# Performance work log

Hardware: AMD Instinct MI355X
Metric: run time of the kernel (lower is better)

## Reference

```python
import jax, jax.numpy as jnp
import numpy as np

B, S, D = 16, 2048, 128

def setup_inputs() -> dict:
    key = jax.random.key(0)
    kq, kk, kv = jax.random.split(key, 3)
    queries = jax.random.normal(kq, (B, S, D), dtype=jnp.float32)
    keys = jax.random.normal(kk, (B, S, D), dtype=jnp.float32)
    values = jax.random.normal(kv, (B, S, D), dtype=jnp.float32)
    return {"queries": queries, "keys": keys, "values": values}

def reference(queries, keys, values):
    # scores: [B, S, S] = Q @ K^T / sqrt(D)
    d = queries.shape[-1]
    scores = jnp.einsum('bqd,bkd->bqk', queries, keys) / jnp.float32(np.sqrt(d))
    attn = jax.nn.softmax(scores, axis=-1)
    # dropout_rate=0.0 -> identity
    out = jnp.einsum('bqk,bkd->bqd', attn, values)
    return out
```

## Files before the change

kernel.cpp:

```cpp
#include <hip/hip_runtime.h>
#include <hip/hip_bf16.h>

#define BATCH 16
#define SEQ   2048
#define DIM   128
#define KTILE 64
#define NIT   (SEQ / KTILE)
#define QT    128
#define SCALE 0.08838834764831845f

typedef __bf16 bf16_t;
typedef __bf16 bf16x8 __attribute__((ext_vector_type(8)));
typedef __bf16 bf16x4 __attribute__((ext_vector_type(4)));
typedef float  f32x4  __attribute__((ext_vector_type(4)));

#define KSTR 136

__device__ __forceinline__ int rho(int s) {
    return (s & 32) | ((s & 4) << 2) | (((s >> 3) & 3) << 2) | (s & 3);
}
__device__ __forceinline__ int swz(int row) {
    return (row & 7) ^ ((row >> 2) & 7);
}

__global__ __launch_bounds__(512, 2)
void attn_fwd(const float* __restrict__ Qg, const float* __restrict__ Kg,
              const float* __restrict__ Vg, float* __restrict__ Og)
{
    __shared__ __align__(16) bf16_t sK [2][KTILE][KSTR];
    __shared__ __align__(16) bf16_t sVt[2][DIM][64];

    const int tid  = threadIdx.x;
    const int wave = tid >> 6;
    const int lane = tid & 63;
    const int l16  = lane & 15;
    const int g    = lane >> 4;
    const bool is_comp = (wave < 4);

    const int bid   = blockIdx.x;
    const int batch = ((bid & 7) << 1) | ((bid >> 7) & 1);
    const int qtile = (bid >> 3) & 15;
    const int q0    = qtile * QT + wave * 32;

    const float* Kb = Kg + (size_t)batch * SEQ * DIM;
    const float* Vb = Vg + (size_t)batch * SEQ * DIM;

    bf16x8 qf[2][4];
    if (is_comp) {
        #pragma unroll
        for (int h = 0; h < 2; ++h) {
            const float* qp =
                Qg + ((size_t)batch * SEQ + q0 + h * 16 + l16) * DIM + g * 8;
            #pragma unroll
            for (int c = 0; c < 4; ++c) {
                const float4 u = *reinterpret_cast<const float4*>(qp + c * 32);
                const float4 v = *reinterpret_cast<const float4*>(qp + c * 32 + 4);
                bf16x8 f;
                f[0] = (bf16_t)(u.x * SCALE); f[1] = (bf16_t)(u.y * SCALE);
                f[2] = (bf16_t)(u.z * SCALE); f[3] = (bf16_t)(u.w * SCALE);
                f[4] = (bf16_t)(v.x * SCALE); f[5] = (bf16_t)(v.y * SCALE);
                f[6] = (bf16_t)(v.z * SCALE); f[7] = (bf16_t)(v.w * SCALE);
                qf[h][c] = f;
            }
        }
    }

    const int p    = tid & 255;
    const int krow = p >> 3;
    const int kch  = p & 7;
    const int vkg  = p >> 5;
    const int vd4  = p & 31;

    float4 ka[2][2][2];
    float4 va[2][4];

    auto load_tile = [&](int k0) {
        #pragma unroll
        for (int r = 0; r < 2; ++r) {
            #pragma unroll
            for (int i = 0; i < 2; ++i) {
                const float* pp =
                    Kb + (size_t)(k0 + krow + r * 32) * DIM + kch * 8 + i * 64;
                ka[r][i][0] = *reinterpret_cast<const float4*>(pp);
                ka[r][i][1] = *reinterpret_cast<const float4*>(pp + 4);
            }
            #pragma unroll
            for (int j = 0; j < 4; ++j)
                va[r][j] = *reinterpret_cast<const float4*>(
                    Vb + (size_t)(k0 + (vkg + r * 8) * 4 + j) * DIM + vd4 * 4);
        }
    };
    auto write_tile = [&](int buf) {
        #pragma unroll
        for (int r = 0; r < 2; ++r) {
            const int row = krow + r * 32;
            #pragma unroll
            for (int i = 0; i < 2; ++i) {
                const float* a = reinterpret_cast<const float*>(&ka[r][i][0]);
                bf16x8 w;
                #pragma unroll
                for (int e = 0; e < 8; ++e) w[e] = (bf16_t)a[e];
                *reinterpret_cast<bf16x8*>(&sK[buf][rho(row)][kch * 8 + i * 64]) = w;
            }
            const int kg = vkg + r * 8;
            #pragma unroll
            for (int dd = 0; dd < 4; ++dd) {
                const int vrow = vd4 * 4 + dd;
                const int col = (((kg >> 1) ^ swz(vrow)) << 3) + ((kg & 1) << 2);
                bf16x4 w;
                w[0] = (bf16_t)va[r][0][dd]; w[1] = (bf16_t)va[r][1][dd];
                w[2] = (bf16_t)va[r][2][dd]; w[3] = (bf16_t)va[r][3][dd];
                *reinterpret_cast<bf16x4*>(&sVt[buf][vrow][col]) = w;
            }
        }
    };

    const f32x4 vzero = {0.f, 0.f, 0.f, 0.f};
    f32x4 o[2][8];
    #pragma unroll
    for (int h = 0; h < 2; ++h)
        #pragma unroll
        for (int i = 0; i < 8; ++i) o[h][i] = vzero;
    float lsum[2] = {0.f, 0.f};

    if (!is_comp) {
        load_tile(0);
        write_tile(0);
        load_tile(KTILE);
    }

    for (int it = 0; it < NIT; ++it) {
        __syncthreads();

        if (!is_comp) {
            if (it + 1 < NIT) {
                write_tile((it + 1) & 1);
                if (it + 2 < NIT) load_tile((it + 2) * KTILE);
            }
            continue;
        }

        const int cur = it & 1;

        f32x4 sc[2][4];
        #pragma unroll
        for (int ksb = 0; ksb < 4; ++ksb) { sc[0][ksb] = vzero; sc[1][ksb] = vzero; }
        #pragma unroll
        for (int c = 0; c < 4; ++c) {
            #pragma unroll
            for (int ksb = 0; ksb < 4; ++ksb) {
                bf16x8 kf = *reinterpret_cast<const bf16x8*>(
                    &sK[cur][ksb * 16 + l16][c * 32 + g * 8]);
                sc[0][ksb] = __builtin_amdgcn_mfma_f32_16x16x32_bf16(
                    kf, qf[0][c], sc[0][ksb], 0, 0, 0);
                sc[1][ksb] = __builtin_amdgcn_mfma_f32_16x16x32_bf16(
                    kf, qf[1][c], sc[1][ksb], 0, 0, 0);
            }
        }

        float pe[2][16];
        #pragma unroll
        for (int h = 0; h < 2; ++h) {
            #pragma unroll
            for (int ksb = 0; ksb < 4; ++ksb) {
                #pragma unroll
                for (int r = 0; r < 4; ++r) {
                    const float pv = __expf(sc[h][ksb][r]);
                    pe[h][ksb * 4 + r] = pv;
                    lsum[h] += pv;
                }
            }
        }
        bf16x8 pb[2][2];
        #pragma unroll
        for (int h = 0; h < 2; ++h) {
            #pragma unroll
            for (int c2 = 0; c2 < 2; ++c2) {
                bf16x8 t;
                #pragma unroll
                for (int jj = 0; jj < 8; ++jj)
                    t[jj] = (bf16_t)pe[h][(2 * c2 + (jj >> 2)) * 4 + (jj & 3)];
                pb[h][c2] = t;
            }
        }

        #pragma unroll
        for (int n0 = 0; n0 < 8; ++n0) {
            const int row = n0 * 16 + l16;
            #pragma unroll
            for (int c2 = 0; c2 < 2; ++c2) {
                bf16x8 vf = *reinterpret_cast<const bf16x8*>(
                    &sVt[cur][row][((c2 * 4 + g) ^ swz(row)) << 3]);
                o[0][n0] = __builtin_amdgcn_mfma_f32_16x16x32_bf16(
                    vf, pb[0][c2], o[0][n0], 0, 0, 0);
                o[1][n0] = __builtin_amdgcn_mfma_f32_16x16x32_bf16(
                    vf, pb[1][c2], o[1][n0], 0, 0, 0);
            }
        }
    }

    if (is_comp) {
        #pragma unroll
        for (int h = 0; h < 2; ++h) {
            float l = lsum[h];
            l += __shfl_xor(l, 16);
            l += __shfl_xor(l, 32);
            const float inv = 1.f / l;
            float* op = Og + ((size_t)batch * SEQ + q0 + h * 16 + l16) * DIM + g * 4;
            #pragma unroll
            for (int n0 = 0; n0 < 8; ++n0) {
                float4 st = { o[h][n0][0] * inv, o[h][n0][1] * inv,
                              o[h][n0][2] * inv, o[h][n0][3] * inv };
                *reinterpret_cast<float4*>(op + n0 * 16) = st;
            }
        }
    }
}

extern "C" void kernel_launch(void* const* d_in, const int* in_sizes, int n_in,
                              void* d_out, int out_size, void* d_ws, size_t ws_size,
                              hipStream_t stream) {
    const float* Q = (const float*)d_in[0];
    const float* K = (const float*)d_in[1];
    const float* V = (const float*)d_in[2];
    float* O = (float*)d_out;
    dim3 grid(BATCH * SEQ / QT);
    dim3 block(512);
    hipLaunchKernelGGL(attn_fwd, grid, block, 0, stream, Q, K, V, O);
}
```

Measured before the change: 127.8 us.

## Quad-buffer K/V tiles, process two tiles per barrier, use exp2 with folded log2e

Shared-memory K/V staging grows from double to quadruple buffering. Producer waves now load and convert two tiles per sync step, and consumer waves process two tiles between barriers, which halves the number of __syncthreads. The softmax scale now folds in log2(e) so exp2f can replace __expf, the row-sum accumulation uses a tree reduction, and s_setprio raises priority around the MFMA blocks. LDS use doubles to about 136KB per block, which may hurt occupancy against the launch_bounds(512,2) target.

```diff
diff --git a/kernel.cpp b/kernel.cpp
--- a/kernel.cpp
+++ b/kernel.cpp
@@ -6,8 +6,9 @@
 #define DIM   128
 #define KTILE 64
 #define NIT   (SEQ / KTILE)
+#define NITP  (NIT / 2)
 #define QT    128
-#define SCALE 0.08838834764831845f
+#define SCALE2 (0.08838834764831845f * 1.4426950408889634f)
 
 typedef __bf16 bf16_t;
 typedef __bf16 bf16x8 __attribute__((ext_vector_type(8)));
@@ -27,8 +28,8 @@
 void attn_fwd(const float* __restrict__ Qg, const float* __restrict__ Kg,
               const float* __restrict__ Vg, float* __restrict__ Og)
 {
-    __shared__ __align__(16) bf16_t sK [2][KTILE][KSTR];
-    __shared__ __align__(16) bf16_t sVt[2][DIM][64];
+    __shared__ __align__(16) bf16_t sK [4][KTILE][KSTR];
+    __shared__ __align__(16) bf16_t sVt[4][DIM][64];
 
     const int tid  = threadIdx.x;
     const int wave = tid >> 6;
@@ -56,10 +57,10 @@
                 const float4 u = *reinterpret_cast<const float4*>(qp + c * 32);
                 const float4 v = *reinterpret_cast<const float4*>(qp + c * 32 + 4);
                 bf16x8 f;
-                f[0] = (bf16_t)(u.x * SCALE); f[1] = (bf16_t)(u.y * SCALE);
-                f[2] = (bf16_t)(u.z * SCALE); f[3] = (bf16_t)(u.w * SCALE);
-                f[4] = (bf16_t)(v.x * SCALE); f[5] = (bf16_t)(v.y * SCALE);
-                f[6] = (bf16_t)(v.z * SCALE); f[7] = (bf16_t)(v.w * SCALE);
+                f[0] = (bf16_t)(u.x * SCALE2); f[1] = (bf16_t)(u.y * SCALE2);
+                f[2] = (bf16_t)(u.z * SCALE2); f[3] = (bf16_t)(u.w * SCALE2);
+                f[4] = (bf16_t)(v.x * SCALE2); f[5] = (bf16_t)(v.y * SCALE2);
+                f[6] = (bf16_t)(v.z * SCALE2); f[7] = (bf16_t)(v.w * SCALE2);
                 qf[h][c] = f;
             }
         }
@@ -71,12 +72,11 @@
     const int vkg  = p >> 5;
     const int vd4  = p & 31;
 
-    float4 ka[2][2][2];
-    float4 va[2][4];
-
-    auto load_tile = [&](int k0) {
-        #pragma unroll
-        for (int r = 0; r < 2; ++r) {
+    auto stage = [&](int k0, int buf) {
+        float4 ka[2][2][2];
+        float4 va[2][4];
+        #pragma unroll
+        for (int r = 0; r < 2; ++r)
             #pragma unroll
             for (int i = 0; i < 2; ++i) {
                 const float* pp =
@@ -84,13 +84,12 @@
                 ka[r][i][0] = *reinterpret_cast<const float4*>(pp);
                 ka[r][i][1] = *reinterpret_cast<const float4*>(pp + 4);
             }
+        #pragma unroll
+        for (int r = 0; r < 2; ++r)
             #pragma unroll
             for (int j = 0; j < 4; ++j)
                 va[r][j] = *reinterpret_cast<const float4*>(
                     Vb + (size_t)(k0 + (vkg + r * 8) * 4 + j) * DIM + vd4 * 4);
-        }
-    };
-    auto write_tile = [&](int buf) {
         #pragma unroll
         for (int r = 0; r < 2; ++r) {
             const int row = krow + r * 32;
@@ -117,85 +116,99 @@
 
     const f32x4 vzero = {0.f, 0.f, 0.f, 0.f};
     f32x4 o[2][8];
-    #pragma unroll
-    for (int h = 0; h < 2; ++h)
-        #pragma unroll
-        for (int i = 0; i < 8; ++i) o[h][i] = vzero;
-    float lsum[2] = {0.f, 0.f};
+    float lsum[2];
+    if (is_comp) {
+        #pragma unroll
+        for (int h = 0; h < 2; ++h) {
+            #pragma unroll
+            for (int i = 0; i < 8; ++i) o[h][i] = vzero;
+            lsum[h] = 0.f;
+        }
+    }
 
     if (!is_comp) {
-        load_tile(0);
-        write_tile(0);
-        load_tile(KTILE);
-    }
-
-    for (int it = 0; it < NIT; ++it) {
+        stage(0, 0);
+        __builtin_amdgcn_sched_barrier(0);
+        stage(KTILE, 1);
+    }
+
+    for (int t = 0; t < NITP; ++t) {
         __syncthreads();
 
         if (!is_comp) {
-            if (it + 1 < NIT) {
-                write_tile((it + 1) & 1);
-                if (it + 2 < NIT) load_tile((it + 2) * KTILE);
+            if (t + 1 < NITP) {
+                stage((2 * t + 2) * KTILE, (2 * t + 2) & 3);
+                __builtin_amdgcn_sched_barrier(0);
+                stage((2 * t + 3) * KTILE, (2 * t + 3) & 3);
             }
             continue;
         }
 
-        const int cur = it & 1;
-
-        f32x4 sc[2][4];
-        #pragma unroll
-        for (int ksb = 0; ksb < 4; ++ksb) { sc[0][ksb] = vzero; sc[1][ksb] = vzero; }
-        #pragma unroll
-        for (int c = 0; c < 4; ++c) {
-            #pragma unroll
-            for (int ksb = 0; ksb < 4; ++ksb) {
-                bf16x8 kf = *reinterpret_cast<const bf16x8*>(
-                    &sK[cur][ksb * 16 + l16][c * 32 + g * 8]);
-                sc[0][ksb] = __builtin_amdgcn_mfma_f32_16x16x32_bf16(
-                    kf, qf[0][c], sc[0][ksb], 0, 0, 0);
-                sc[1][ksb] = __builtin_amdgcn_mfma_f32_16x16x32_bf16(
-                    kf, qf[1][c], sc[1][ksb], 0, 0, 0);
-            }
-        }
-
-        float pe[2][16];
-        #pragma unroll
-        for (int h = 0; h < 2; ++h) {
-            #pragma unroll
-            for (int ksb = 0; ksb < 4; ++ksb) {
-                #pragma unroll
-                for (int r = 0; r < 4; ++r) {
-                    const float pv = __expf(sc[h][ksb][r]);
-                    pe[h][ksb * 4 + r] = pv;
-                    lsum[h] += pv;
+        #pragma unroll
+        for (int s = 0; s < 2; ++s) {
+            const int cur = (2 * t + s) & 3;
+
+            f32x4 sc[2][4];
+            #pragma unroll
+            for (int ksb = 0; ksb < 4; ++ksb) { sc[0][ksb] = vzero; sc[1][ksb] = vzero; }
+            __builtin_amdgcn_s_setprio(1);
+            #pragma unroll
+            for (int c = 0; c < 4; ++c) {
+                #pragma unroll
+                for (int ksb = 0; ksb < 4; ++ksb) {
+                    bf16x8 kf = *reinterpret_cast<const bf16x8*>(
+                        &sK[cur][ksb * 16 + l16][c * 32 + g * 8]);
+                    sc[0][ksb] = __builtin_amdgcn_mfma_f32_16x16x32_bf16(
+                        kf, qf[0][c], sc[0][ksb], 0, 0, 0);
+                    sc[1][ksb] = __builtin_amdgcn_mfma_f32_16x16x32_bf16(
+                        kf, qf[1][c], sc[1][ksb], 0, 0, 0);
                 }
             }
-        }
-        bf16x8 pb[2][2];
-        #pragma unroll
-        for (int h = 0; h < 2; ++h) {
-            #pragma unroll
-            for (int c2 = 0; c2 < 2; ++c2) {
-                bf16x8 t;
-                #pragma unroll
-                for (int jj = 0; jj < 8; ++jj)
-                    t[jj] = (bf16_t)pe[h][(2 * c2 + (jj >> 2)) * 4 + (jj & 3)];
-                pb[h][c2] = t;
-            }
-        }
-
-        #pragma unroll
-        for (int n0 = 0; n0 < 8; ++n0) {
-            const int row = n0 * 16 + l16;
-            #pragma unroll
-            for (int c2 = 0; c2 < 2; ++c2) {
-                bf16x8 vf = *reinterpret_cast<const bf16x8*>(
-                    &sVt[cur][row][((c2 * 4 + g) ^ swz(row)) << 3]);
-                o[0][n0] = __builtin_amdgcn_mfma_f32_16x16x32_bf16(
-                    vf, pb[0][c2], o[0][n0], 0, 0, 0);
-                o[1][n0] = __builtin_amdgcn_mfma_f32_16x16x32_bf16(
-                    vf, pb[1][c2], o[1][n0], 0, 0, 0);
-            }
+            __builtin_amdgcn_s_setprio(0);
+
+            float pe[2][16];
+            #pragma unroll
+            for (int h = 0; h < 2; ++h)
+                #pragma unroll
+                for (int ksb = 0; ksb < 4; ++ksb)
+                    #pragma unroll
+                    for (int r = 0; r < 4; ++r)
+                        pe[h][ksb * 4 + r] = exp2f(sc[h][ksb][r]);
+            #pragma unroll
+            for (int h = 0; h < 2; ++h) {
+                const float s0 = (pe[h][0] + pe[h][1]) + (pe[h][2] + pe[h][3]);
+                const float s1 = (pe[h][4] + pe[h][5]) + (pe[h][6] + pe[h][7]);
+                const float s2 = (pe[h][8] + pe[h][9]) + (pe[h][10] + pe[h][11]);
+                const float s3 = (pe[h][12] + pe[h][13]) + (pe[h][14] + pe[h][15]);
+                lsum[h] += (s0 + s1) + (s2 + s3);
+            }
+            bf16x8 pb[2][2];
+            #pragma unroll
+            for (int h = 0; h < 2; ++h)
+                #pragma unroll
+                for (int c2 = 0; c2 < 2; ++c2) {
+                    bf16x8 tt;
+                    #pragma unroll
+                    for (int jj = 0; jj < 8; ++jj)
+                        tt[jj] = (bf16_t)pe[h][(2 * c2 + (jj >> 2)) * 4 + (jj & 3)];
+                    pb[h][c2] = tt;
+                }
+
+            __builtin_amdgcn_s_setprio(1);
+            #pragma unroll
+            for (int n0 = 0; n0 < 8; ++n0) {
+                const int row = n0 * 16 + l16;
+                #pragma unroll
+                for (int c2 = 0; c2 < 2; ++c2) {
+                    bf16x8 vf = *reinterpret_cast<const bf16x8*>(
+                        &sVt[cur][row][((c2 * 4 + g) ^ swz(row)) << 3]);
+                    o[0][n0] = __builtin_amdgcn_mfma_f32_16x16x32_bf16(
+                        vf, pb[0][c2], o[0][n0], 0, 0, 0);
+                    o[1][n0] = __builtin_amdgcn_mfma_f32_16x16x32_bf16(
+                        vf, pb[1][c2], o[1][n0], 0, 0, 0);
+                }
+            }
+            __builtin_amdgcn_s_setprio(0);
         }
     }
 
```

New measurement: 127.9 us. Within noise of the previous version (+0.1%).
